# Kernel optimization log

Hardware: AMD Instinct MI355X
Metric: run time of the kernel (lower is better)

The kernel has to match this reference:

```python
import jax, jax.numpy as jnp
import numpy as np

N_NODES = 100000
N_PAIRS = 1600000
F = 64
H = 4
D = F // H  # head dim = 16


def setup_inputs() -> dict:
    key = jax.random.key(0)
    ks = jax.random.split(key, 9)
    x = jax.random.normal(ks[0], (N_NODES, F), dtype=jnp.float32)
    w_ij = jax.random.normal(ks[1], (N_PAIRS, F), dtype=jnp.float32)
    phi_r_cut = jax.random.uniform(ks[2], (N_PAIRS,), dtype=jnp.float32)
    pair_mask = jnp.ones((N_PAIRS,), dtype=jnp.float32)
    Wq = jax.random.normal(ks[3], (H, D, D), dtype=jnp.float32) / np.sqrt(D)
    Wk = jax.random.normal(ks[4], (H, D, D), dtype=jnp.float32) / np.sqrt(D)
    Wv = jax.random.normal(ks[5], (H, D, D), dtype=jnp.float32) / np.sqrt(D)
    idx_i = jnp.sort(jax.random.randint(ks[6], (N_PAIRS,), 0, N_NODES)).astype(jnp.int64)
    idx_j = jax.random.randint(ks[7], (N_PAIRS,), 0, N_NODES).astype(jnp.int64)
    return {"x": x, "w_ij": w_ij, "phi_r_cut": phi_r_cut, "pair_mask": pair_mask,
            "Wq": Wq, "Wk": Wk, "Wv": Wv, "idx_i": idx_i, "idx_j": idx_j}


def reference(x, w_ij, phi_r_cut, pair_mask, Wq, Wk, Wv, idx_i, idx_j):
    n, f = x.shape
    h, d, _ = Wq.shape
    xh = x.reshape(n, h, d)            # (n, H, D) head split
    wh = w_ij.reshape(-1, h, d)        # (p, H, D)
    # per-head projections (Dense with no bias: x @ kernel), then gather by edge
    q_i = jnp.einsum('nhd,hde->nhe', xh, Wq)[idx_i]   # (p, H, D)
    k_j = jnp.einsum('nhd,hde->nhe', xh, Wk)[idx_j]   # (p, H, D)
    alpha = (q_i * wh * k_j).sum(axis=-1) / jnp.sqrt(jnp.asarray(d, x.dtype))  # (p, H)
    alpha = alpha * (pair_mask * phi_r_cut)[:, None]  # safe_scale with cutoff * mask
    v_j = jnp.einsum('nhd,hde->nhe', xh, Wv)[idx_j]   # (p, H, D)
    out = jax.ops.segment_sum(alpha[..., None] * v_j, idx_i, num_segments=n)  # (n, H, D)
    return out.reshape(n, f)
```

## Files before the change

### kernel.cpp

```cpp
#include <hip/hip_runtime.h>
#include <hip/hip_fp16.h>
#include <stdint.h>

#define N_NODES_C 100000
#define N_PAIRS_C 1600000
#define FDIM 64
#define HH 4
#define DD 16

typedef float vf4 __attribute__((ext_vector_type(4)));

__global__ __launch_bounds__(256) void qkv_kernel(
    const float* __restrict__ x,
    const float* __restrict__ Wq,
    const float* __restrict__ Wk,
    const float* __restrict__ Wv,
    float* __restrict__ q,
    __half* __restrict__ kv)
{
    __shared__ float sWq[HH][DD * DD + 8];
    __shared__ float sWk[HH][DD * DD + 8];
    __shared__ float sWv[HH][DD * DD + 8];
    for (int t = threadIdx.x; t < HH * DD * DD; t += 256) {
        sWq[t >> 8][t & 255] = Wq[t];
        sWk[t >> 8][t & 255] = Wk[t];
        sWv[t >> 8][t & 255] = Wv[t];
    }
    __syncthreads();

    int gid = blockIdx.x * 256 + threadIdx.x;
    int n = gid >> 2;
    int h = gid & 3;
    if (n >= N_NODES_C) return;

    const float* xp = x + (int64_t)n * FDIM + h * DD;
    float xr[DD];
#pragma unroll
    for (int d0 = 0; d0 < DD; d0 += 4) {
        float4 t4 = *reinterpret_cast<const float4*>(xp + d0);
        xr[d0 + 0] = t4.x; xr[d0 + 1] = t4.y; xr[d0 + 2] = t4.z; xr[d0 + 3] = t4.w;
    }

    float qo[DD], ko[DD], vo[DD];
#pragma unroll
    for (int e = 0; e < DD; e++) { qo[e] = 0.f; ko[e] = 0.f; vo[e] = 0.f; }

    const float* wqh = sWq[h];
    const float* wkh = sWk[h];
    const float* wvh = sWv[h];
#pragma unroll
    for (int d = 0; d < DD; d++) {
        float xv = xr[d];
#pragma unroll
        for (int e = 0; e < DD; e++) {
            qo[e] = fmaf(xv, wqh[d * DD + e], qo[e]);
            ko[e] = fmaf(xv, wkh[d * DD + e], ko[e]);
            vo[e] = fmaf(xv, wvh[d * DD + e], vo[e]);
        }
    }

    int64_t qbase = (int64_t)n * FDIM + h * DD;
#pragma unroll
    for (int e0 = 0; e0 < DD; e0 += 4) {
        *reinterpret_cast<float4*>(q + qbase + e0) = make_float4(qo[e0], qo[e0+1], qo[e0+2], qo[e0+3]);
    }

    __half2 kvh[DD];
#pragma unroll
    for (int e = 0; e < DD; e++) kvh[e] = __floats2half2_rn(ko[e], vo[e]);
    uint4* dst = reinterpret_cast<uint4*>(kv + (int64_t)n * 128 + h * 32);
    const uint4* src = reinterpret_cast<const uint4*>(kvh);
#pragma unroll
    for (int t = 0; t < 4; t++) dst[t] = src[t];
}

__global__ __launch_bounds__(256) void pair_kernel(
    const float* __restrict__ q,
    const __half* __restrict__ kv,
    const float* __restrict__ w_ij,
    const float* __restrict__ phi,
    const float* __restrict__ mask,
    const int*  __restrict__ idx_i,
    const int*  __restrict__ idx_j,
    float* __restrict__ out,
    int pairs_per_group)
{
    int gid = blockIdx.x * 256 + threadIdx.x;
    int grp = gid >> 4;
    int m   = threadIdx.x & 15;

    int64_t start = (int64_t)grp * pairs_per_group;
    if (start >= N_PAIRS_C) return;
    int64_t end = start + pairs_per_group;
    if (end > N_PAIRS_C) end = N_PAIRS_C;

    const vf4*   w4p = reinterpret_cast<const vf4*>(w_ij);
    const float4* q4p = reinterpret_cast<const float4*>(q);

    int64_t p1 = (start + 1 < end) ? start + 1 : end - 1;
    int   i_a = idx_i[start];
    int   j_a = idx_j[start];
    float s_a = phi[start] * mask[start];
    int   i_b = idx_i[p1];
    int   j_b = idx_j[p1];
    float s_b = phi[p1] * mask[p1];

    vf4   w_a  = __builtin_nontemporal_load(w4p + start * DD + m);
    uint4 kv_a = *reinterpret_cast<const uint4*>(kv + (int64_t)j_a * 128 + m * 8);

    float4 q4  = q4p[(int64_t)i_a * DD + m];
    int cur_i  = i_a;
    float4 acc = make_float4(0.f, 0.f, 0.f, 0.f);

    for (int64_t p = start; p < end; ++p) {
        int64_t p2 = (p + 2 < end) ? p + 2 : end - 1;
        int   i_c = idx_i[p2];
        int   j_c = idx_j[p2];
        float s_c = phi[p2] * mask[p2];

        int64_t pn = (p + 1 < end) ? p + 1 : end - 1;
        vf4   w_b  = __builtin_nontemporal_load(w4p + pn * DD + m);
        uint4 kv_b = *reinterpret_cast<const uint4*>(kv + (int64_t)j_b * 128 + m * 8);

        if (i_a != cur_i) {
            int64_t ob = (int64_t)cur_i * FDIM + m * 4;
            atomicAdd(&out[ob + 0], acc.x);
            atomicAdd(&out[ob + 1], acc.y);
            atomicAdd(&out[ob + 2], acc.z);
            atomicAdd(&out[ob + 3], acc.w);
            acc = make_float4(0.f, 0.f, 0.f, 0.f);
            q4 = q4p[(int64_t)i_a * DD + m];
            cur_i = i_a;
        }

        const __half2* hp = reinterpret_cast<const __half2*>(&kv_a);
        float2 e0 = __half22float2(hp[0]);
        float2 e1 = __half22float2(hp[1]);
        float2 e2 = __half22float2(hp[2]);
        float2 e3 = __half22float2(hp[3]);

        float r = q4.x * w_a.x * e0.x
                + q4.y * w_a.y * e1.x
                + q4.z * w_a.z * e2.x
                + q4.w * w_a.w * e3.x;
        r += __shfl_xor(r, 1);
        r += __shfl_xor(r, 2);
        float alpha = r * 0.25f * s_a;

        acc.x = fmaf(alpha, e0.y, acc.x);
        acc.y = fmaf(alpha, e1.y, acc.y);
        acc.z = fmaf(alpha, e2.y, acc.z);
        acc.w = fmaf(alpha, e3.y, acc.w);

        i_a = i_b; j_a = j_b; s_a = s_b;
        w_a = w_b; kv_a = kv_b;
        i_b = i_c; j_b = j_c; s_b = s_c;
    }

    {
        int64_t ob = (int64_t)cur_i * FDIM + m * 4;
        atomicAdd(&out[ob + 0], acc.x);
        atomicAdd(&out[ob + 1], acc.y);
        atomicAdd(&out[ob + 2], acc.z);
        atomicAdd(&out[ob + 3], acc.w);
    }
}

extern "C" void kernel_launch(void* const* d_in, const int* in_sizes, int n_in,
                              void* d_out, int out_size, void* d_ws, size_t ws_size,
                              hipStream_t stream) {
    const float* x       = (const float*)d_in[0];
    const float* w_ij    = (const float*)d_in[1];
    const float* phi     = (const float*)d_in[2];
    const float* mask    = (const float*)d_in[3];
    const float* Wq      = (const float*)d_in[4];
    const float* Wk      = (const float*)d_in[5];
    const float* Wv      = (const float*)d_in[6];
    const int*   idx_i   = (const int*)d_in[7];
    const int*   idx_j   = (const int*)d_in[8];
    float* out = (float*)d_out;

    float*  q  = (float*)d_ws;
    __half* kv = (__half*)(q + (int64_t)N_NODES_C * FDIM);

    hipMemsetAsync(d_out, 0, (size_t)out_size * sizeof(float), stream);

    int qkv_blocks = (N_NODES_C * HH + 255) / 256;
    qkv_kernel<<<qkv_blocks, 256, 0, stream>>>(x, Wq, Wk, Wv, q, kv);

    const int n_groups = 32768;
    int pairs_per_group = (N_PAIRS_C + n_groups - 1) / n_groups;
    pair_kernel<<<n_groups / 16, 256, 0, stream>>>(q, kv, w_ij, phi, mask,
                                                   idx_i, idx_j, out, pairs_per_group);
}
```

Before: 672.4 us.

## Fuse output zeroing into QKV kernel, deepen w prefetch, use 32-bit indexing

```diff
diff --git a/kernel.cpp b/kernel.cpp
--- a/kernel.cpp
+++ b/kernel.cpp
@@ -16,7 +16,8 @@
     const float* __restrict__ Wk,
     const float* __restrict__ Wv,
     float* __restrict__ q,
-    __half* __restrict__ kv)
+    __half* __restrict__ kv,
+    float* __restrict__ out)
 {
     __shared__ float sWq[HH][DD * DD + 8];
     __shared__ float sWk[HH][DD * DD + 8];
@@ -33,12 +34,13 @@
     int h = gid & 3;
     if (n >= N_NODES_C) return;
 
-    const float* xp = x + (int64_t)n * FDIM + h * DD;
+    const vf4* xp4 = reinterpret_cast<const vf4*>(x + (int64_t)n * FDIM + h * DD);
     float xr[DD];
 #pragma unroll
-    for (int d0 = 0; d0 < DD; d0 += 4) {
-        float4 t4 = *reinterpret_cast<const float4*>(xp + d0);
-        xr[d0 + 0] = t4.x; xr[d0 + 1] = t4.y; xr[d0 + 2] = t4.z; xr[d0 + 3] = t4.w;
+    for (int d0 = 0; d0 < 4; d0++) {
+        vf4 t4 = __builtin_nontemporal_load(xp4 + d0);
+        xr[d0 * 4 + 0] = t4.x; xr[d0 * 4 + 1] = t4.y;
+        xr[d0 * 4 + 2] = t4.z; xr[d0 * 4 + 3] = t4.w;
     }
 
     float qo[DD], ko[DD], vo[DD];
@@ -60,9 +62,12 @@
     }
 
     int64_t qbase = (int64_t)n * FDIM + h * DD;
+    float4 z4 = make_float4(0.f, 0.f, 0.f, 0.f);
 #pragma unroll
     for (int e0 = 0; e0 < DD; e0 += 4) {
-        *reinterpret_cast<float4*>(q + qbase + e0) = make_float4(qo[e0], qo[e0+1], qo[e0+2], qo[e0+3]);
+        *reinterpret_cast<float4*>(q + qbase + e0) =
+            make_float4(qo[e0], qo[e0+1], qo[e0+2], qo[e0+3]);
+        *reinterpret_cast<float4*>(out + qbase + e0) = z4;
     }
 
     __half2 kvh[DD];
@@ -89,47 +94,52 @@
     int grp = gid >> 4;
     int m   = threadIdx.x & 15;
 
-    int64_t start = (int64_t)grp * pairs_per_group;
+    int start = grp * pairs_per_group;
     if (start >= N_PAIRS_C) return;
-    int64_t end = start + pairs_per_group;
+    int end = start + pairs_per_group;
     if (end > N_PAIRS_C) end = N_PAIRS_C;
 
-    const vf4*   w4p = reinterpret_cast<const vf4*>(w_ij);
-    const float4* q4p = reinterpret_cast<const float4*>(q);
-
-    int64_t p1 = (start + 1 < end) ? start + 1 : end - 1;
-    int   i_a = idx_i[start];
-    int   j_a = idx_j[start];
-    float s_a = phi[start] * mask[start];
-    int   i_b = idx_i[p1];
-    int   j_b = idx_j[p1];
-    float s_b = phi[p1] * mask[p1];
-
-    vf4   w_a  = __builtin_nontemporal_load(w4p + start * DD + m);
-    uint4 kv_a = *reinterpret_cast<const uint4*>(kv + (int64_t)j_a * 128 + m * 8);
-
-    float4 q4  = q4p[(int64_t)i_a * DD + m];
+    const vf4*    w4p  = reinterpret_cast<const vf4*>(w_ij);
+    const float4* q4p  = reinterpret_cast<const float4*>(q);
+    const uint4*  kv4p = reinterpret_cast<const uint4*>(kv);
+
+    int p1 = (start + 1 < end) ? start + 1 : end - 1;
+    int   i_a = __builtin_nontemporal_load(idx_i + start);
+    int   j_a = __builtin_nontemporal_load(idx_j + start);
+    float s_a = __builtin_nontemporal_load(phi + start)
+              * __builtin_nontemporal_load(mask + start) * 0.25f;
+    int   i_b = __builtin_nontemporal_load(idx_i + p1);
+    int   j_b = __builtin_nontemporal_load(idx_j + p1);
+    float s_b = __builtin_nontemporal_load(phi + p1)
+              * __builtin_nontemporal_load(mask + p1) * 0.25f;
+
+    vf4   w_a  = __builtin_nontemporal_load(w4p + (((uint32_t)start) << 4) + m);
+    vf4   w_b  = __builtin_nontemporal_load(w4p + (((uint32_t)p1)    << 4) + m);
+    uint4 kv_a = kv4p[(((uint32_t)j_a) << 4) + m];
+
+    float4 q4  = q4p[(((uint32_t)i_a) << 4) + m];
     int cur_i  = i_a;
     float4 acc = make_float4(0.f, 0.f, 0.f, 0.f);
 
-    for (int64_t p = start; p < end; ++p) {
-        int64_t p2 = (p + 2 < end) ? p + 2 : end - 1;
-        int   i_c = idx_i[p2];
-        int   j_c = idx_j[p2];
-        float s_c = phi[p2] * mask[p2];
-
-        int64_t pn = (p + 1 < end) ? p + 1 : end - 1;
-        vf4   w_b  = __builtin_nontemporal_load(w4p + pn * DD + m);
-        uint4 kv_b = *reinterpret_cast<const uint4*>(kv + (int64_t)j_b * 128 + m * 8);
+    for (int p = start; p < end; ++p) {
+        int p2 = (p + 2 < end) ? p + 2 : end - 1;
+
+        int   i_c = __builtin_nontemporal_load(idx_i + p2);
+        int   j_c = __builtin_nontemporal_load(idx_j + p2);
+        float s_c = __builtin_nontemporal_load(phi + p2)
+                  * __builtin_nontemporal_load(mask + p2) * 0.25f;
+        vf4   w_c = __builtin_nontemporal_load(w4p + (((uint32_t)p2) << 4) + m);
+
+        uint4 kv_b = kv4p[(((uint32_t)j_b) << 4) + m];
 
         if (i_a != cur_i) {
-            int64_t ob = (int64_t)cur_i * FDIM + m * 4;
+            uint32_t ob = (((uint32_t)cur_i) << 6) + (m << 2);
             atomicAdd(&out[ob + 0], acc.x);
             atomicAdd(&out[ob + 1], acc.y);
             atomicAdd(&out[ob + 2], acc.z);
             atomicAdd(&out[ob + 3], acc.w);
             acc = make_float4(0.f, 0.f, 0.f, 0.f);
-            q4 = q4p[(int64_t)i_a * DD + m];
+            q4 = q4p[(((uint32_t)i_a) << 4) + m];
             cur_i = i_a;
         }
 
@@ -145,7 +155,7 @@
                 + q4.w * w_a.w * e3.x;
         r += __shfl_xor(r, 1);
         r += __shfl_xor(r, 2);
-        float alpha = r * 0.25f * s_a;
+        float alpha = r * s_a;
 
         acc.x = fmaf(alpha, e0.y, acc.x);
         acc.y = fmaf(alpha, e1.y, acc.y);
@@ -153,12 +163,12 @@
         acc.w = fmaf(alpha, e3.y, acc.w);
 
         i_a = i_b; j_a = j_b; s_a = s_b;
-        w_a = w_b; kv_a = kv_b;
         i_b = i_c; j_b = j_c; s_b = s_c;
+        w_a = w_b; w_b = w_c; kv_a = kv_b;
     }
 
     {
-        int64_t ob = (int64_t)cur_i * FDIM + m * 4;
+        uint32_t ob = (((uint32_t)cur_i) << 6) + (m << 2);
         atomicAdd(&out[ob + 0], acc.x);
         atomicAdd(&out[ob + 1], acc.y);
         atomicAdd(&out[ob + 2], acc.z);
@@ -183,10 +193,8 @@
     float*  q  = (float*)d_ws;
     __half* kv = (__half*)(q + (int64_t)N_NODES_C * FDIM);
 
-    hipMemsetAsync(d_out, 0, (size_t)out_size * sizeof(float), stream);
-
     int qkv_blocks = (N_NODES_C * HH + 255) / 256;
-    qkv_kernel<<<qkv_blocks, 256, 0, stream>>>(x, Wq, Wk, Wv, q, kv);
+    qkv_kernel<<<qkv_blocks, 256, 0, stream>>>(x, Wq, Wk, Wv, q, kv, out);
 
     const int n_groups = 32768;
     int pairs_per_group = (N_PAIRS_C + n_groups - 1) / n_groups;
```

After: 742.5 us. 1.1x slower.
